# Kernel optimization log

Hardware: AMD Instinct MI355X
Metric: run time of the kernel (lower is better)

## Reference

```python
import jax, jax.numpy as jnp
import numpy as np

B, S, E, H, D, NE, R = 2, 2048, 2048, 16, 128, 8, 16
HALF = D // 2
THETA = 10000.0


def setup_inputs() -> dict:
    key = jax.random.key(0)
    ks = jax.random.split(key, 18)

    def w(k, shape, fan_in):
        return jax.random.normal(k, shape, jnp.float32) / np.float32(np.sqrt(fan_in))

    inp = {
        "x": jax.random.normal(ks[0], (B, S, E), jnp.float32),
        "expert_mask": jax.random.uniform(ks[1], (B, S, NE), dtype=jnp.float32),
    }
    for i, n in enumerate(("q", "k", "v")):
        inp["W" + n] = w(ks[2 + 3 * i], (H * D, E), E)
        inp["b" + n] = jnp.zeros((H * D,), jnp.float32)
        inp["A" + n] = w(ks[3 + 3 * i], (NE, R, E), E)
        inp["B" + n] = w(ks[4 + 3 * i], (H * D, NE, R), R)
    inp["Wo"] = w(ks[11], (E, H * D), H * D)
    inp["bo"] = jnp.zeros((E,), jnp.float32)
    inp["Ao"] = w(ks[12], (NE, R, H * D), H * D)
    inp["Bo"] = w(ks[13], (E, NE, R), R)
    return inp


def routed_linear(x, W, b, A, Bm, mask):
    """MaybeRoutedLinear: dense base + expert-routed low-rank path gated by mask [B,S,NE]."""
    y = jnp.einsum("bsi,oi->bso", x, W) + b
    h = jnp.einsum("bsi,eri->bser", x, A) * mask[..., None]  # [B,S,NE,R]
    return y + jnp.einsum("bser,oer->bso", h, Bm)


def apply_rope(t):
    """Llama-style rotary embedding. t: [B,S,H,D]."""
    inv_freq = 1.0 / (THETA ** (jnp.arange(0, D, 2, dtype=jnp.float32) / D))  # [D/2]
    freqs = jnp.arange(S, dtype=jnp.float32)[:, None] * inv_freq[None, :]  # [S,D/2]
    cos = jnp.concatenate([jnp.cos(freqs)] * 2, -1)[None, :, None, :]  # [1,S,1,D]
    sin = jnp.concatenate([jnp.sin(freqs)] * 2, -1)[None, :, None, :]
    rot = jnp.concatenate([-t[..., HALF:], t[..., :HALF]], -1)
    return t * cos + rot * sin


def reference(x, expert_mask, Wq, bq, Aq, Bq, Wk, bk, Ak, Bk, Wv, bv, Av, Bv, Wo, bo, Ao, Bo):
    q = routed_linear(x, Wq, bq, Aq, Bq, expert_mask).reshape(B, S, H, D)
    k = routed_linear(x, Wk, bk, Ak, Bk, expert_mask).reshape(B, S, H, D)
    v = routed_linear(x, Wv, bv, Av, Bv, expert_mask).reshape(B, S, H, D)
    q = apply_rope(q)
    k = apply_rope(k)
    scores = jnp.einsum("bqhd,bkhd->bhqk", q, k) / jnp.float32(np.sqrt(D))
    causal = jnp.tril(jnp.ones((S, S), dtype=bool))
    scores = jnp.where(causal[None, None], scores, jnp.finfo(scores.dtype).min)
    probs = jax.nn.softmax(scores, axis=-1)
    o = jnp.einsum("bhqk,bkhd->bqhd", probs, v).reshape(B, S, H * D)
    return routed_linear(o, Wo, bo, Ao, Bo, expert_mask)
```

## Files before the change

kernel.cpp:

```cpp
#include <hip/hip_runtime.h>


#define B_ 2
#define S_ 2048
#define E_ 2048
#define H_ 16
#define D_ 128
#define NE_ 8
#define R_ 16
#define HD_ 2048
#define M_ 4096
#define KL_ 128

typedef unsigned short u16;
typedef unsigned int u32;
typedef __attribute__((ext_vector_type(8))) short bf16x8;
typedef __attribute__((ext_vector_type(4))) float f32x4;

typedef const __attribute__((address_space(1))) void gvoid_t;
typedef __attribute__((address_space(3))) void svoid_t;

__device__ __forceinline__ float bf2f(u16 u) {
    union { u32 i; float f; } v; v.i = ((u32)u) << 16; return v.f;
}
__device__ __forceinline__ u16 f2bf(float f) {
    union { float f; u32 i; } v; v.f = f;
    u32 x = v.i;
    return (u16)((x + 0x7fffu + ((x >> 16) & 1u)) >> 16);
}
__device__ __forceinline__ float ldf(const void* p, size_t i, int f) {
    return f ? ((const float*)p)[i] : bf2f(((const u16*)p)[i]);
}
__device__ __forceinline__ float4 ld4(const void* p, size_t i, int f) {
    if (f) return *(const float4*)((const float*)p + i);
    ushort4 v = *(const ushort4*)((const u16*)p + i);
    return make_float4(bf2f(v.x), bf2f(v.y), bf2f(v.z), bf2f(v.w));
}

__global__ void k_detect(const void* __restrict__ x, int* __restrict__ flags) {
    __shared__ int votes[2];
    int tid = threadIdx.x;
    if (tid < 2) votes[tid] = 0;
    __syncthreads();
    const u32* p = (const u32*)x;
    int bad = 0, tot = 0;
    for (int i = tid; i < 4096; i += 64) {
        u32 lo = p[i] & 0xffffu;
        if (lo) {
            tot++;
            int e = (int)((lo >> 7) & 0xffu);
            if (e < 100 || e > 150) bad++;
        }
    }
    atomicAdd(&votes[0], bad);
    atomicAdd(&votes[1], tot);
    __syncthreads();
    if (tid == 0) flags[0] = (votes[1] > 0 && votes[0] * 10 > votes[1] * 3) ? 1 : 0;
}

__global__ void k_cvt(const void* __restrict__ src, u16* __restrict__ dst, int n,
                      const int* __restrict__ flags) {
    int fin = flags[0];
    int i = (blockIdx.x * 256 + threadIdx.x) * 4;
    if (i >= n) return;
    float4 v = ld4(src, i, fin);
    ushort4 o;
    o.x = f2bf(v.x); o.y = f2bf(v.y); o.z = f2bf(v.z); o.w = f2bf(v.w);
    *(ushort4*)(dst + i) = o;
}

#define NX_  8388608L
#define NA1_ 262144L
#define NW_  4194304L
__global__ void k_cvt_all(
    const void* __restrict__ x,
    const void* __restrict__ Aq, const void* __restrict__ Ak,
    const void* __restrict__ Av, const void* __restrict__ Ao,
    const void* __restrict__ Bq, const void* __restrict__ Bk,
    const void* __restrict__ Bv, const void* __restrict__ Bo,
    const void* __restrict__ Wq, const void* __restrict__ Wk,
    const void* __restrict__ Wv,
    u16* __restrict__ Xb, u16* __restrict__ Acat, u16* __restrict__ Bmcat,
    u16* __restrict__ Wqb, u16* __restrict__ Wkb, u16* __restrict__ Wvb,
    const int* __restrict__ flags) {
    int fin = flags[0];
    long i = (long)(blockIdx.x * 256 + threadIdx.x) * 4;
    const void* src; u16* dst; long off;
    if (i < NX_) { src = x; dst = Xb; off = i; }
    else if (i < NX_ + 4 * NA1_) {
        long j = i - NX_; int p = (int)(j >> 18); off = j & (NA1_ - 1);
        src = (p == 0) ? Aq : (p == 1) ? Ak : (p == 2) ? Av : Ao;
        dst = Acat + (long)p * NA1_;
    } else if (i < NX_ + 8 * NA1_) {
        long j = i - NX_ - 4 * NA1_; int p = (int)(j >> 18); off = j & (NA1_ - 1);
        src = (p == 0) ? Bq : (p == 1) ? Bk : (p == 2) ? Bv : Bo;
        dst = Bmcat + (long)p * NA1_;
    } else {
        long j = i - NX_ - 8 * NA1_; int p = (int)(j / NW_); off = j - (long)p * NW_;
        src = (p == 0) ? Wq : (p == 1) ? Wk : Wv;
        dst = (p == 0) ? Wqb : (p == 1) ? Wkb : Wvb;
    }
    float4 v = ld4(src, off, fin);
    ushort4 o;
    o.x = f2bf(v.x); o.y = f2bf(v.y); o.z = f2bf(v.z); o.w = f2bf(v.w);
    *(ushort4*)(dst + off) = o;
}

#define BM_ 128
#define BN_ 128
#define BK_ 64

__global__ __launch_bounds__(256, 2) void k_gemm_mfma(
    const u16* __restrict__ A, int lda,
    const u16* __restrict__ Bw, int ldb, int K1,
    const u16* __restrict__ A2, int lda2,
    const u16* __restrict__ B2, int K2,
    const void* __restrict__ bias, const void* __restrict__ mask,
    void* __restrict__ C, int ldc, int store_mode,
    const int* __restrict__ flags) {
    __shared__ __align__(16) u16 As[BM_ * BK_];
    __shared__ __align__(16) u16 Bs[BN_ * BK_];
    int fin = flags[0];
    int tid = threadIdx.x;
    int w = tid >> 6, lane = tid & 63;
    int l15 = lane & 15, quad = lane >> 4;
    int wm = w >> 1, wn = w & 1;
    int m0 = blockIdx.y * BM_, n0 = blockIdx.x * BN_;
    int lrow = lane >> 3;
    int lcol = (lane & 7) * 8;

    f32x4 acc[4][4];
#pragma unroll
    for (int mt = 0; mt < 4; mt++)
#pragma unroll
        for (int nt = 0; nt < 4; nt++)
#pragma unroll
            for (int r = 0; r < 4; r++) acc[mt][nt][r] = 0.f;

    int n1 = K1 / BK_, n2 = K2 / BK_;
    int total = n1 + n2;
    for (int it = 0; it < total; it++) {
        const u16 *pa, *pb; int sa, sb, kb;
        if (it < n1) { pa = A;  sa = lda;  pb = Bw; sb = ldb; kb = it * BK_; }
        else         { pa = A2; sa = lda2; pb = B2; sb = K2;  kb = (it - n1) * BK_; }
        __syncthreads();
#pragma unroll
        for (int i = 0; i < 4; i++) {
            int rowb = (w * 4 + i) * 8;
            int r = rowb + lrow;
            __builtin_amdgcn_global_load_lds(
                (gvoid_t*)(pa + (size_t)(m0 + r) * sa + kb + lcol),
                (svoid_t*)(As + rowb * BK_), 16, 0, 0);
            __builtin_amdgcn_global_load_lds(
                (gvoid_t*)(pb + (size_t)(n0 + r) * sb + kb + lcol),
                (svoid_t*)(Bs + rowb * BK_), 16, 0, 0);
        }
        __syncthreads();
#pragma unroll
        for (int kk = 0; kk < 2; kk++) {
            int ko = kk * 32 + quad * 8;
            bf16x8 af[4], bf[4];
#pragma unroll
            for (int mt = 0; mt < 4; mt++)
                af[mt] = *(const bf16x8*)(As + (wm * 64 + mt * 16 + l15) * BK_ + ko);
#pragma unroll
            for (int nt = 0; nt < 4; nt++)
                bf[nt] = *(const bf16x8*)(Bs + (wn * 64 + nt * 16 + l15) * BK_ + ko);
#pragma unroll
            for (int mt = 0; mt < 4; mt++)
#pragma unroll
                for (int nt = 0; nt < 4; nt++)
                    acc[mt][nt] = __builtin_amdgcn_mfma_f32_16x16x32_bf16(
                        af[mt], bf[nt], acc[mt][nt], 0, 0, 0);
        }
    }

#pragma unroll
    for (int mt = 0; mt < 4; mt++) {
#pragma unroll
        for (int r = 0; r < 4; r++) {
            int m = m0 + wm * 64 + mt * 16 + quad * 4 + r;
#pragma unroll
            for (int nt = 0; nt < 4; nt++) {
                int n = n0 + wn * 64 + nt * 16 + l15;
                float v = acc[mt][nt][r];
                if (bias) v += ldf(bias, (size_t)n, fin);
                if (mask) v *= ldf(mask, (size_t)m * NE_ + ((n & 127) >> 4), fin);
                int f32out = (store_mode == 2) ? fin : store_mode;
                if (f32out) ((float*)C)[(size_t)m * ldc + n] = v;
                else        ((u16*)C)[(size_t)m * ldc + n] = f2bf(v);
            }
        }
    }
}

__global__ void k_rope2(u16* __restrict__ Q, u16* __restrict__ K) {
    const int n = M_ * HD_ / 2;
    int idx = blockIdx.x * 256 + threadIdx.x;
    u16* Y = (idx < n) ? Q : K;
    int id = (idx < n) ? idx : idx - n;
    int d2 = id & 63;
    int sh = id >> 6;
    int s = (sh >> 4) & (S_ - 1);
    float inv = powf(10000.f, -(float)d2 * (1.f / 64.f));
    float fr = (float)s * inv;
    float c, sn;
    sincosf(fr, &sn, &c);
    size_t base = ((size_t)sh) << 7;
    float t0 = bf2f(Y[base + d2]);
    float t1 = bf2f(Y[base + d2 + 64]);
    Y[base + d2]      = f2bf(t0 * c - t1 * sn);
    Y[base + d2 + 64] = f2bf(t1 * c + t0 * sn);
}

__global__ void k_transpose_v(const u16* __restrict__ Vb, u16* __restrict__ Vt) {
    __shared__ u16 t[32][33];
    int s0 = blockIdx.x * 32;
    int n0 = blockIdx.y * 32;
    int b  = blockIdx.z;
    int tx = threadIdx.x & 31, ty = threadIdx.x >> 5;
#pragma unroll
    for (int r = 0; r < 4; r++)
        t[ty + r * 8][tx] = Vb[((size_t)(b * S_ + s0 + ty + r * 8)) * HD_ + n0 + tx];
    __syncthreads();
#pragma unroll
    for (int r = 0; r < 4; r++)
        Vt[((size_t)(b * HD_ + n0 + ty + r * 8)) * S_ + s0 + tx] = t[tx][ty + r * 8];
}

#define KS_ST 136
#define VT_ST 72
#define SCALE_ 0.088388347648318447f

__global__ __launch_bounds__(256, 3) void k_flash4(
    const u16* __restrict__ Q, const u16* __restrict__ K,
    const u16* __restrict__ Vt, u16* __restrict__ O) {
    __shared__ __align__(16) u16 Ks[64 * KS_ST];
    __shared__ __align__(16) u16 Vs[128 * VT_ST];
    __shared__ __align__(16) u16 Ps[64 * VT_ST];
    int tid = threadIdx.x;
    int w = tid >> 6, lane = tid & 63;
    int l15 = lane & 15, quad = lane >> 4;
    int bh = blockIdx.y, b = bh >> 4, h = bh & 15;
    int t = 31 - blockIdx.x;
    int q0 = t * 64;

    int krow[4], kd8[4], vd[4], vkg[4];
#pragma unroll
    for (int it = 0; it < 4; it++) {
        int idx = it * 256 + tid;
        krow[it] = idx >> 4; kd8[it] = (idx & 15) * 8;
        vd[it] = idx >> 3;   vkg[it] = (idx & 7) * 8;
    }

    bf16x8 qf[4];
    size_t baseQ = ((size_t)(b * S_ + q0 + w * 16 + l15)) * HD_ + h * D_;
#pragma unroll
    for (int ks = 0; ks < 4; ks++)
        qf[ks] = *(const bf16x8*)(Q + baseQ + ks * 32 + quad * 8);

    f32x4 of[8];
#pragma unroll
    for (int nt = 0; nt < 8; nt++)
#pragma unroll
        for (int r = 0; r < 4; r++) of[nt][r] = 0.f;
    float mrow[4], lrow[4];
#pragma unroll
    for (int r = 0; r < 4; r++) { mrow[r] = -30000.f; lrow[r] = 0.f; }

    int nch = t + 1;

    bf16x8 kpre[4], vpre[4];
#pragma unroll
    for (int it = 0; it < 4; it++) {
        kpre[it] = *(const bf16x8*)(K + ((size_t)(b * S_ + krow[it])) * HD_ + h * D_ + kd8[it]);
        vpre[it] = *(const bf16x8*)(Vt + ((size_t)(bh * 128 + vd[it])) * S_ + vkg[it]);
    }

    for (int c = 0; c < nch; c++) {
        int k0 = c * 64;
        __syncthreads();
#pragma unroll
        for (int it = 0; it < 4; it++) {
            *(bf16x8*)(Ks + krow[it] * KS_ST + kd8[it]) = kpre[it];
            *(bf16x8*)(Vs + vd[it] * VT_ST + vkg[it]) = vpre[it];
        }
        __syncthreads();
        if (c + 1 < nch) {
            int k1 = k0 + 64;
#pragma unroll
            for (int it = 0; it < 4; it++) {
                kpre[it] = *(const bf16x8*)(K + ((size_t)(b * S_ + k1 + krow[it])) * HD_ + h * D_ + kd8[it]);
                vpre[it] = *(const bf16x8*)(Vt + ((size_t)(bh * 128 + vd[it])) * S_ + k1 + vkg[it]);
            }
        }

        f32x4 sf[4];
#pragma unroll
        for (int nt = 0; nt < 4; nt++)
#pragma unroll
            for (int r = 0; r < 4; r++) sf[nt][r] = 0.f;
#pragma unroll
        for (int ks = 0; ks < 4; ks++) {
            int koff = ks * 32 + quad * 8;
            bf16x8 qa = qf[ks];
#pragma unroll
            for (int nt = 0; nt < 4; nt++) {
                bf16x8 kb = *(const bf16x8*)(Ks + (nt * 16 + l15) * KS_ST + koff);
                sf[nt] = __builtin_amdgcn_mfma_f32_16x16x32_bf16(qa, kb, sf[nt], 0, 0, 0);
            }
        }

        int rowb = q0 + w * 16 + quad * 4;
        float al[4];
#pragma unroll
        for (int nt = 0; nt < 4; nt++) {
            int key = k0 + nt * 16 + l15;
#pragma unroll
            for (int r = 0; r < 4; r++) {
                float sv = sf[nt][r] * SCALE_;
                sf[nt][r] = (key > rowb + r) ? -30000.f : sv;
            }
        }
#pragma unroll
        for (int r = 0; r < 4; r++) {
            float cmax = fmaxf(fmaxf(sf[0][r], sf[1][r]), fmaxf(sf[2][r], sf[3][r]));
            cmax = fmaxf(cmax, __shfl_xor(cmax, 1, 64));
            cmax = fmaxf(cmax, __shfl_xor(cmax, 2, 64));
            cmax = fmaxf(cmax, __shfl_xor(cmax, 4, 64));
            cmax = fmaxf(cmax, __shfl_xor(cmax, 8, 64));
            float mnew = fmaxf(mrow[r], cmax);
            float a = __expf(mrow[r] - mnew);
            mrow[r] = mnew;
            al[r] = a;
            float psum = 0.f;
#pragma unroll
            for (int nt = 0; nt < 4; nt++) {
                float p = __expf(sf[nt][r] - mnew);
                sf[nt][r] = p;
                psum += p;
            }
            psum += __shfl_xor(psum, 1, 64);
            psum += __shfl_xor(psum, 2, 64);
            psum += __shfl_xor(psum, 4, 64);
            psum += __shfl_xor(psum, 8, 64);
            lrow[r] = lrow[r] * a + psum;
        }
#pragma unroll
        for (int nt = 0; nt < 4; nt++)
#pragma unroll
            for (int r = 0; r < 4; r++)
                Ps[(w * 16 + quad * 4 + r) * VT_ST + nt * 16 + l15] = f2bf(sf[nt][r]);
#pragma unroll
        for (int nt = 0; nt < 8; nt++)
#pragma unroll
            for (int r = 0; r < 4; r++) of[nt][r] *= al[r];

#pragma unroll
        for (int ks2 = 0; ks2 < 2; ks2++) {
            int koff = ks2 * 32 + quad * 8;
            bf16x8 pa = *(const bf16x8*)(Ps + (w * 16 + l15) * VT_ST + koff);
#pragma unroll
            for (int nt = 0; nt < 8; nt++) {
                bf16x8 vb = *(const bf16x8*)(Vs + (nt * 16 + l15) * VT_ST + koff);
                of[nt] = __builtin_amdgcn_mfma_f32_16x16x32_bf16(pa, vb, of[nt], 0, 0, 0);
            }
        }
    }

    int rowb = q0 + w * 16 + quad * 4;
#pragma unroll
    for (int r = 0; r < 4; r++) {
        float inv = 1.f / lrow[r];
        size_t base = ((size_t)(b * S_ + rowb + r)) * HD_ + h * D_;
#pragma unroll
        for (int nt = 0; nt < 8; nt++)
            O[base + nt * 16 + l15] = f2bf(of[nt][r] * inv);
    }
}

extern "C" void kernel_launch(void* const* d_in, const int* in_sizes, int n_in,
                              void* d_out, int out_size, void* d_ws, size_t ws_size,
                              hipStream_t stream) {
    const void* x    = d_in[0];
    const void* mask = d_in[1];
    const void* Wq = d_in[2];  const void* bq = d_in[3];
    const void* Aq = d_in[4];  const void* Bq = d_in[5];
    const void* Wk = d_in[6];  const void* bk = d_in[7];
    const void* Ak = d_in[8];  const void* Bk = d_in[9];
    const void* Wv = d_in[10]; const void* bv = d_in[11];
    const void* Av = d_in[12]; const void* Bv = d_in[13];
    const void* Wo = d_in[14]; const void* bo = d_in[15];
    const void* Ao = d_in[16]; const void* Bo = d_in[17];

    char* ws = (char*)d_ws;
    const long MB = 1 << 20;
    int* flags = (int*)ws;
    u16* Xb    = (u16*)(ws + 1  * MB);
    u16* Acat  = (u16*)(ws + 17 * MB);
    u16* Bmcat = (u16*)(ws + 19 * MB);
    u16* hg3   = (u16*)(ws + 21 * MB);
    u16* hgo   = (u16*)(ws + 24 * MB);
    u16* Qb    = (u16*)(ws + 25 * MB);
    u16* Kb    = (u16*)(ws + 41 * MB);
    u16* Vb    = (u16*)(ws + 57 * MB);
    u16* Vt    = (u16*)(ws + 73 * MB);
    u16* Wqb   = Kb;
    u16* Wkb   = Vb;
    u16* Wvb   = Vt;
    u16* Wob   = Qb;
    u16* Ob    = Vb;

    k_detect<<<1, 64, 0, stream>>>(x, flags);
    const long NCVT = NX_ + 8 * NA1_ + 3 * NW_;
    k_cvt_all<<<NCVT / 1024, 256, 0, stream>>>(
        x, Aq, Ak, Av, Ao, Bq, Bk, Bv, Bo, Wq, Wk, Wv,
        Xb, Acat, Bmcat, Wqb, Wkb, Wvb, flags);

    k_gemm_mfma<<<dim3(3, M_ / BM_), 256, 0, stream>>>(
        Xb, E_, Acat, E_, E_, nullptr, 0, nullptr, 0,
        nullptr, mask, hg3, 384, 0, flags);

    dim3 gg(HD_ / BN_, M_ / BM_);
    k_gemm_mfma<<<gg, 256, 0, stream>>>(Xb, E_, Wqb, E_, E_, hg3 + 0,   384, Bmcat, KL_,
                                        bq, nullptr, Qb, HD_, 0, flags);
    k_gemm_mfma<<<gg, 256, 0, stream>>>(Xb, E_, Wkb, E_, E_, hg3 + 128, 384, Bmcat + NA1_, KL_,
                                        bk, nullptr, Kb, HD_, 0, flags);
    k_gemm_mfma<<<gg, 256, 0, stream>>>(Xb, E_, Wvb, E_, E_, hg3 + 256, 384, Bmcat + 2 * NA1_, KL_,
                                        bv, nullptr, Vb, HD_, 0, flags);

    k_rope2<<<(M_ * HD_) / 256, 256, 0, stream>>>(Qb, Kb);
    k_transpose_v<<<dim3(S_ / 32, HD_ / 32, B_), 256, 0, stream>>>(Vb, Vt);

    k_flash4<<<dim3(32, 32), 256, 0, stream>>>(Qb, Kb, Vt, Ob);

    k_cvt<<<NW_ / 1024, 256, 0, stream>>>(Wo, Wob, (int)NW_, flags);
    k_gemm_mfma<<<dim3(1, M_ / BM_), 256, 0, stream>>>(
        Ob, HD_, Acat + 3 * NA1_, E_, E_, nullptr, 0, nullptr, 0,
        nullptr, mask, hgo, KL_, 0, flags);
    k_gemm_mfma<<<gg, 256, 0, stream>>>(Ob, HD_, Wob, E_, E_, hgo, KL_, Bmcat + 3 * NA1_, KL_,
                                        bo, nullptr, d_out, HD_, 2, flags);
}
```

Baseline: 761.9 us.

## Read K/V directly from global in flash attention and swizzle blocks across XCDs

The flash attention kernel no longer stages K and V tiles through shared memory with register prefetch and two barriers per chunk. Each wave now loads its MFMA operands straight from global memory and relies on the L1/L2 caches for reuse across the four waves. Blocks are remapped so that blocks of the same batch-head land together on one XCD, and the occupancy hint rises from 3 to 4 blocks per CU. This removes barrier and LDS traffic but exposes global load latency and multiplies cache requests, since the software prefetch is gone.

```diff
diff --git a/kernel.cpp b/kernel.cpp
--- a/kernel.cpp
+++ b/kernel.cpp
@@ -228,30 +228,25 @@
         Vt[((size_t)(b * HD_ + n0 + ty + r * 8)) * S_ + s0 + tx] = t[tx][ty + r * 8];
 }
 
-#define KS_ST 136
 #define VT_ST 72
 #define SCALE_ 0.088388347648318447f
 
-__global__ __launch_bounds__(256, 3) void k_flash4(
+__global__ __launch_bounds__(256, 4) void k_flash5(
     const u16* __restrict__ Q, const u16* __restrict__ K,
     const u16* __restrict__ Vt, u16* __restrict__ O) {
-    __shared__ __align__(16) u16 Ks[64 * KS_ST];
-    __shared__ __align__(16) u16 Vs[128 * VT_ST];
     __shared__ __align__(16) u16 Ps[64 * VT_ST];
     int tid = threadIdx.x;
     int w = tid >> 6, lane = tid & 63;
     int l15 = lane & 15, quad = lane >> 4;
-    int bh = blockIdx.y, b = bh >> 4, h = bh & 15;
-    int t = 31 - blockIdx.x;
+
+    int lin = blockIdx.y * 32 + blockIdx.x;
+    int wg  = (lin & 7) * 128 + (lin >> 3);
+    int bh = wg >> 5, b = bh >> 4, h = bh & 15;
+    int t = 31 - (wg & 31);
     int q0 = t * 64;
 
-    int krow[4], kd8[4], vd[4], vkg[4];
-#pragma unroll
-    for (int it = 0; it < 4; it++) {
-        int idx = it * 256 + tid;
-        krow[it] = idx >> 4; kd8[it] = (idx & 15) * 8;
-        vd[it] = idx >> 3;   vkg[it] = (idx & 7) * 8;
-    }
+    const u16* Kb = K  + (size_t)(b * S_) * HD_ + h * D_;
+    const u16* Vb = Vt + (size_t)(bh * 128) * S_;
 
     bf16x8 qf[4];
     size_t baseQ = ((size_t)(b * S_ + q0 + w * 16 + l15)) * HD_ + h * D_;
@@ -269,31 +264,8 @@
     for (int r = 0; r < 4; r++) { mrow[r] = -30000.f; lrow[r] = 0.f; }
 
     int nch = t + 1;
-
-    bf16x8 kpre[4], vpre[4];
-#pragma unroll
-    for (int it = 0; it < 4; it++) {
-        kpre[it] = *(const bf16x8*)(K + ((size_t)(b * S_ + krow[it])) * HD_ + h * D_ + kd8[it]);
-        vpre[it] = *(const bf16x8*)(Vt + ((size_t)(bh * 128 + vd[it])) * S_ + vkg[it]);
-    }
-
     for (int c = 0; c < nch; c++) {
         int k0 = c * 64;
-        __syncthreads();
-#pragma unroll
-        for (int it = 0; it < 4; it++) {
-            *(bf16x8*)(Ks + krow[it] * KS_ST + kd8[it]) = kpre[it];
-            *(bf16x8*)(Vs + vd[it] * VT_ST + vkg[it]) = vpre[it];
-        }
-        __syncthreads();
-        if (c + 1 < nch) {
-            int k1 = k0 + 64;
-#pragma unroll
-            for (int it = 0; it < 4; it++) {
-                kpre[it] = *(const bf16x8*)(K + ((size_t)(b * S_ + k1 + krow[it])) * HD_ + h * D_ + kd8[it]);
-                vpre[it] = *(const bf16x8*)(Vt + ((size_t)(bh * 128 + vd[it])) * S_ + k1 + vkg[it]);
-            }
-        }
 
         f32x4 sf[4];
 #pragma unroll
@@ -306,7 +278,7 @@
             bf16x8 qa = qf[ks];
 #pragma unroll
             for (int nt = 0; nt < 4; nt++) {
-                bf16x8 kb = *(const bf16x8*)(Ks + (nt * 16 + l15) * KS_ST + koff);
+                bf16x8 kb = *(const bf16x8*)(Kb + (size_t)(k0 + nt * 16 + l15) * HD_ + koff);
                 sf[nt] = __builtin_amdgcn_mfma_f32_16x16x32_bf16(qa, kb, sf[nt], 0, 0, 0);
             }
         }
@@ -362,7 +334,7 @@
             bf16x8 pa = *(const bf16x8*)(Ps + (w * 16 + l15) * VT_ST + koff);
 #pragma unroll
             for (int nt = 0; nt < 8; nt++) {
-                bf16x8 vb = *(const bf16x8*)(Vs + (nt * 16 + l15) * VT_ST + koff);
+                bf16x8 vb = *(const bf16x8*)(Vb + (size_t)(nt * 16 + l15) * S_ + k0 + koff);
                 of[nt] = __builtin_amdgcn_mfma_f32_16x16x32_bf16(pa, vb, of[nt], 0, 0, 0);
             }
         }
@@ -432,7 +404,7 @@
     k_rope2<<<(M_ * HD_) / 256, 256, 0, stream>>>(Qb, Kb);
     k_transpose_v<<<dim3(S_ / 32, HD_ / 32, B_), 256, 0, stream>>>(Vb, Vt);
 
-    k_flash4<<<dim3(32, 32), 256, 0, stream>>>(Qb, Kb, Vt, Ob);
+    k_flash5<<<dim3(32, 32), 256, 0, stream>>>(Qb, Kb, Vt, Ob);
 
     k_cvt<<<NW_ / 1024, 256, 0, stream>>>(Wo, Wob, (int)NW_, flags);
     k_gemm_mfma<<<dim3(1, M_ / BM_), 256, 0, stream>>>(
```

Measured after the change: 1.031 ms. +35.4%, slower.
